# Optimization experiments

Measured on AMD Instinct MI355X. Metric: run time of the kernel, lower is better.

Reference implementation:

```python
import jax, jax.numpy as jnp
import numpy as np

NUM_HEADS = 16
EPS = 1e-5

def _lif(z, vth=1.0):
    # MyNode with fresh membrane and a single call: out = (0/tau + z >= vth)
    return (z >= vth).astype(z.dtype)

def _bn(z, g, b):
    # BatchNorm1d in train mode on (M, C, N): batch stats over (M, N)
    mu = z.mean(axis=(0, 2), keepdims=True)
    var = ((z - mu) ** 2).mean(axis=(0, 2), keepdims=True)
    return g[None, :, None] * (z - mu) * jax.lax.rsqrt(var + EPS) + b[None, :, None]

def _conv1(z, w, bias=None):
    # 1x1 Conv1d: (M, C, N) x (D, C) -> (M, D, N)
    out = jnp.einsum('mcn,dc->mdn', z, w)
    if bias is not None:
        out = out + bias[None, :, None]
    return out

def _rpb_matrix(P, N):
    # vectorized SCA_VA.compute_RPB_matrix: B[i*W+j, k*W+l] = P[(i-k)+M-1, (j-l)+M-1]
    Hs = int(round(N ** 0.5)); M = Hs + 1
    d = jnp.arange(Hs)[:, None] - jnp.arange(Hs)[None, :] + (M - 1)  # (Hs, Hs)
    Bm = P[d[:, None, :, None], d[None, :, None, :]]  # [i, j, k, l]
    return Bm.reshape(N, N)

def _sca(x, y, W, G, Bt, rpb=None):
    # shared body of SCA_AV / SCA_VA; W:(4,C,C) = [q,k,v,proj], G/Bt:(4,C) BN affine
    T, B, C, N = x.shape
    H = NUM_HEADS; D = C // H
    xf = x.reshape(T * B, C, N); yf = y.reshape(T * B, C, N)
    def branch(src, i):
        s = _lif(_bn(_conv1(src, W[i]), G[i], Bt[i]))  # (TB, C, N) binary spikes
        return s.reshape(T, B, C, N).transpose(0, 1, 3, 2).reshape(T, B, N, H, D).transpose(0, 1, 3, 2, 4)
    q = branch(xf, 0)  # (T,B,H,N,D)
    k = branch(yf, 1)
    v = branch(yf, 2)
    attn = jnp.einsum('tbhnd,tbhmd->tbhnm', q, k)  # no softmax: raw spike q@k^T
    if rpb is not None:
        attn = _lif(attn + rpb[None, None, None])  # rpb_lif (v_threshold=1.0)
    o = jnp.einsum('tbhnm,tbhmd->tbhnd', attn, v) * 0.25  # self.scale = 0.25
    o = o.transpose(0, 1, 2, 4, 3).reshape(T, B, C, N)
    o = _lif(o.reshape(T * B, C, N), 0.5)  # attn_lif v_threshold=0.5
    o = _lif(_bn(_conv1(o, W[3]), G[3], Bt[3]))  # proj_conv + proj_bn + proj_lif
    return o.reshape(T, B, C, N)

def _forward(x, y, av_w, av_g, av_b, va_w, va_g, va_b, P_rpb,
             fc1_w, fc1_b, fc2_w, fc2_b,
             m1_w, m1_b, m1_g, m1_bb, m2_w, m2_b, m2_g, m2_bb):
    T, B, C, N = x.shape
    # cross-modal spiking attention (visual->audio and audio->visual)
    x1 = x + _sca(x, y, av_w, av_g, av_b)                       # SCA_AV(x, y)
    y1 = y + _sca(y, x, va_w, va_g, va_b, rpb=_rpb_matrix(P_rpb, N))  # SCA_VA(y, x)
    # CMCI fusion: Linear on channel dim of transposed tensors, then LIF
    zx = jnp.einsum('tbcn,dc->tbdn', x1, fc1_w) + fc1_b[None, None, :, None]
    zy = jnp.einsum('tbcn,dc->tbdn', y1, fc2_w) + fc2_b[None, None, :, None]
    cur = _lif(zx + zy)  # (T,B,C,N)
    # MLPBlock: residual MLP (conv1x1 -> BN -> LIF) x 2
    cf = cur.reshape(T * B, C, N)
    h = _lif(_bn(_conv1(cf, m1_w, m1_b), m1_g, m1_bb))
    o = _lif(_bn(_conv1(h, m2_w, m2_b), m2_g, m2_bb))
    return cur + o.reshape(T, B, C, N)

def setup_inputs() -> dict:
    key = jax.random.key(0)
    ks = jax.random.split(key, 16)
    T, B, C, N = 4, 8, 256, 196
    Hd = 4 * C
    M2 = 2 * (int(N ** 0.5) + 1) - 1  # 29
    s = 0.05
    return {
        'x': jax.random.normal(ks[0], (T, B, C, N), jnp.float32),
        'y': jax.random.normal(ks[1], (T, B, C, N), jnp.float32),
        'av_w': jax.random.normal(ks[2], (4, C, C), jnp.float32) * s,
        'av_g': jnp.ones((4, C), jnp.float32),
        'av_b': jnp.zeros((4, C), jnp.float32),
        'va_w': jax.random.normal(ks[3], (4, C, C), jnp.float32) * s,
        'va_g': jnp.ones((4, C), jnp.float32),
        'va_b': jnp.zeros((4, C), jnp.float32),
        'P_rpb': jax.random.normal(ks[4], (M2, M2), jnp.float32),
        'fc1_w': jax.random.normal(ks[5], (C, C), jnp.float32) * s,
        'fc1_b': jnp.zeros((C,), jnp.float32),
        'fc2_w': jax.random.normal(ks[6], (C, C), jnp.float32) * s,
        'fc2_b': jnp.zeros((C,), jnp.float32),
        'm1_w': jax.random.normal(ks[7], (Hd, C), jnp.float32) * s,
        'm1_b': jnp.zeros((Hd,), jnp.float32),
        'm1_g': jnp.ones((Hd,), jnp.float32),
        'm1_bb': jnp.zeros((Hd,), jnp.float32),
        'm2_w': jax.random.normal(ks[8], (C, Hd), jnp.float32) * s,
        'm2_b': jnp.zeros((C,), jnp.float32),
        'm2_g': jnp.ones((C,), jnp.float32),
        'm2_bb': jnp.zeros((C,), jnp.float32),
    }

def reference(x, y, av_w, av_g, av_b, va_w, va_g, va_b, P_rpb,
              fc1_w, fc1_b, fc2_w, fc2_b,
              m1_w, m1_b, m1_g, m1_bb, m2_w, m2_b, m2_g, m2_bb):
    return _forward(x, y, av_w, av_g, av_b, va_w, va_g, va_b, P_rpb,
                    fc1_w, fc1_b, fc2_w, fc2_b,
                    m1_w, m1_b, m1_g, m1_bb, m2_w, m2_b, m2_g, m2_bb)
```

## Files before the change

kernel.cpp:

```cpp
#include <hip/hip_runtime.h>
#include <math.h>

#define TBB 32
#define CC  256
#define NN  196
#define NJ  (TBB * NN)
#define HD  1024
#define SLAB   ((size_t)TBB * CC * NN)
#define SLAB1K ((size_t)TBB * HD * NN)

struct Ptr6  { const float* p[6]; };
struct PtrM6 { float*       p[6]; };

__global__ __launch_bounds__(256) void gemm_tile(
    const float* __restrict__ W,  const float* __restrict__ In,
    const float* __restrict__ W2, const float* __restrict__ In2,
    const float* __restrict__ bias, const float* __restrict__ bias2,
    float* __restrict__ Z, int Cout, int Cin)
{
    __shared__ float As[16][64];
    __shared__ float Bs[16][64];
    const int t  = threadIdx.x;
    const int tx = t & 15, ty = t >> 4;
    const int d0 = blockIdx.x * 64;
    const int j0 = blockIdx.y * 64;

    float acc[4][4] = {{0.f}};

    const int wrow = t >> 2;
    const int wk   = (t & 3) * 4;
    const int skk  = t >> 4;
    const int sj   = (t & 15) * 4;

    size_t inoff[4];
    {
        int jb = j0 + sj;
        #pragma unroll
        for (int i = 0; i < 4; ++i) {
            int j = jb + i;
            int m = j / NN;
            int n = j - m * NN;
            inoff[i] = (size_t)m * Cin * NN + n;
        }
    }

    for (int pass = 0; pass < 2; ++pass) {
        const float* Wp = pass ? W2 : W;
        const float* Ip = pass ? In2 : In;
        if (Wp == nullptr) break;
        for (int k0 = 0; k0 < Cin; k0 += 16) {
            float4 w4 = *(const float4*)(Wp + (size_t)(d0 + wrow) * Cin + (k0 + wk));
            float bvals[4];
            #pragma unroll
            for (int i = 0; i < 4; ++i)
                bvals[i] = Ip[inoff[i] + (size_t)(k0 + skk) * NN];

            As[wk + 0][wrow] = w4.x;
            As[wk + 1][wrow] = w4.y;
            As[wk + 2][wrow] = w4.z;
            As[wk + 3][wrow] = w4.w;
            #pragma unroll
            for (int i = 0; i < 4; ++i) Bs[skk][sj + i] = bvals[i];
            __syncthreads();

            #pragma unroll
            for (int kk = 0; kk < 16; ++kk) {
                float4 a4 = *(const float4*)(&As[kk][ty * 4]);
                float4 b4 = *(const float4*)(&Bs[kk][tx * 4]);
                float ar[4] = {a4.x, a4.y, a4.z, a4.w};
                float br[4] = {b4.x, b4.y, b4.z, b4.w};
                #pragma unroll
                for (int i = 0; i < 4; ++i)
                    #pragma unroll
                    for (int jj = 0; jj < 4; ++jj)
                        acc[i][jj] = fmaf(ar[i], br[jj], acc[i][jj]);
            }
            __syncthreads();
        }
    }

    #pragma unroll
    for (int i = 0; i < 4; ++i) {
        int d = d0 + ty * 4 + i;
        float bv = 0.f;
        if (bias)  bv += bias[d];
        if (bias2) bv += bias2[d];
        #pragma unroll
        for (int jj = 0; jj < 4; ++jj) {
            int j = j0 + tx * 4 + jj;
            int m = j / NN;
            int n = j - m * NN;
            Z[(size_t)(m * Cout + d) * NN + n] = acc[i][jj] + bv;
        }
    }
}

__global__ __launch_bounds__(256) void bn_stats(
    Ptr6 Zs, Ptr6 gs, Ptr6 bs, int Cout,
    float* __restrict__ scale, float* __restrict__ shift)
{
    const int d = blockIdx.x, g = blockIdx.y, t = threadIdx.x;
    const float* Z = Zs.p[g];
    double s = 0.0, s2 = 0.0;
    for (int i = t; i < NJ; i += 256) {
        int m = i / NN, n = i - m * NN;
        double v = (double)Z[(size_t)(m * Cout + d) * NN + n];
        s += v; s2 += v * v;
    }
    __shared__ double sh[256], sh2[256];
    sh[t] = s; sh2[t] = s2;
    __syncthreads();
    for (int off = 128; off > 0; off >>= 1) {
        if (t < off) { sh[t] += sh[t + off]; sh2[t] += sh2[t + off]; }
        __syncthreads();
    }
    if (t == 0) {
        double mu  = sh[0] / (double)NJ;
        double var = sh2[0] / (double)NJ - mu * mu;
        double a   = (double)gs.p[g][d] / sqrt(var + 1e-5);
        scale[g * Cout + d] = (float)a;
        shift[g * Cout + d] = (float)((double)bs.p[g][d] - mu * a);
    }
}

__global__ __launch_bounds__(256) void bn_apply(
    Ptr6 Zs, PtrM6 Ss, const float* __restrict__ scale,
    const float* __restrict__ shift, int Cout, int total)
{
    int g = blockIdx.y;
    int idx = blockIdx.x * 256 + threadIdx.x;
    if (idx >= total) return;
    int d = (idx / NN) % Cout;
    float v = fmaf(scale[g * Cout + d], Zs.p[g][idx], shift[g * Cout + d]);
    Ss.p[g][idx] = (v >= 1.f) ? 1.f : 0.f;
}

__global__ __launch_bounds__(256) void attention_k(
    const float* __restrict__ Q, const float* __restrict__ K,
    const float* __restrict__ V, const float* __restrict__ P,
    float* __restrict__ O)
{
    const int m = blockIdx.x;
    const int h = blockIdx.y;
    const int t = threadIdx.x;
    __shared__ unsigned int qb[196], kb[196], vb[196];
    __shared__ float Pl[841];

    if (P) { for (int i = t; i < 841; i += 256) Pl[i] = P[i]; }
    if (t < 196) {
        unsigned int q = 0, k = 0, v = 0;
        size_t base = (size_t)m * CC * NN + (size_t)h * 16 * NN + t;
        #pragma unroll
        for (int dd = 0; dd < 16; ++dd) {
            size_t off = base + (size_t)dd * NN;
            if (Q[off] > 0.5f) q |= (1u << dd);
            if (K[off] > 0.5f) k |= (1u << dd);
            if (V[off] > 0.5f) v |= (1u << dd);
        }
        qb[t] = q; kb[t] = k; vb[t] = v;
    }
    __syncthreads();

    if (t < 196) {
        int acc[16] = {0};
        const int ni = t / 14, nj = t - ni * 14;
        const unsigned int qr = qb[t];
        if (P) {
            for (int mm = 0; mm < 196; ++mm) {
                int a = __popc(qr & kb[mm]);
                int mi = mm / 14, mj = mm - mi * 14;
                float sv = (float)a + Pl[(ni - mi + 14) * 29 + (nj - mj + 14)];
                if (sv >= 1.f) {
                    unsigned int vv = vb[mm];
                    #pragma unroll
                    for (int dd = 0; dd < 16; ++dd)
                        acc[dd] += (vv >> dd) & 1;
                }
            }
        } else {
            for (int mm = 0; mm < 196; ++mm) {
                int a = __popc(qr & kb[mm]);
                if (a) {
                    unsigned int vv = vb[mm];
                    #pragma unroll
                    for (int dd = 0; dd < 16; ++dd)
                        acc[dd] += ((vv >> dd) & 1) ? a : 0;
                }
            }
        }
        size_t base = (size_t)m * CC * NN + (size_t)h * 16 * NN + t;
        #pragma unroll
        for (int dd = 0; dd < 16; ++dd)
            O[base + (size_t)dd * NN] = (acc[dd] >= 2) ? 1.f : 0.f;
    }
}

__global__ __launch_bounds__(256) void add_residual2(
    const float* __restrict__ x, const float* __restrict__ y,
    const float* __restrict__ sx, const float* __restrict__ sy,
    float* __restrict__ X1, float* __restrict__ Y1)
{
    size_t i = (size_t)blockIdx.x * 256 + threadIdx.x;
    if (i >= SLAB) return;
    X1[i] = x[i] + sx[i];
    Y1[i] = y[i] + sy[i];
}

__global__ __launch_bounds__(256) void lif1(
    const float* __restrict__ Z, float* __restrict__ S, int total)
{
    int i = blockIdx.x * 256 + threadIdx.x;
    if (i >= total) return;
    S[i] = (Z[i] >= 1.f) ? 1.f : 0.f;
}

__global__ __launch_bounds__(256) void final_add(
    const float* __restrict__ cur, const float* __restrict__ o,
    float* __restrict__ out, int total)
{
    int i = blockIdx.x * 256 + threadIdx.x;
    if (i >= total) return;
    out[i] = cur[i] + o[i];
}

extern "C" void kernel_launch(void* const* d_in, const int* in_sizes, int n_in,
                              void* d_out, int out_size, void* d_ws, size_t ws_size,
                              hipStream_t stream)
{
    const float* x     = (const float*)d_in[0];
    const float* y     = (const float*)d_in[1];
    const float* av_w  = (const float*)d_in[2];
    const float* av_g  = (const float*)d_in[3];
    const float* av_b  = (const float*)d_in[4];
    const float* va_w  = (const float*)d_in[5];
    const float* va_g  = (const float*)d_in[6];
    const float* va_b  = (const float*)d_in[7];
    const float* P_rpb = (const float*)d_in[8];
    const float* fc1_w = (const float*)d_in[9];
    const float* fc1_b = (const float*)d_in[10];
    const float* fc2_w = (const float*)d_in[11];
    const float* fc2_b = (const float*)d_in[12];
    const float* m1_w  = (const float*)d_in[13];
    const float* m1_b  = (const float*)d_in[14];
    const float* m1_g  = (const float*)d_in[15];
    const float* m1_bb = (const float*)d_in[16];
    const float* m2_w  = (const float*)d_in[17];
    const float* m2_b  = (const float*)d_in[18];
    const float* m2_g  = (const float*)d_in[19];
    const float* m2_bb = (const float*)d_in[20];
    float* out = (float*)d_out;

    float* ws    = (float*)d_ws;
    float* A     = ws;
    float* Bf    = A  + 6 * SLAB;
    float* Cf    = Bf + 2 * SLAB;
    float* scale = Cf + 2 * SLAB;
    float* shift = scale + 6 * 1024;

    const size_t CC2 = (size_t)CC * CC;
    const int blocksSlab  = (int)(SLAB / 256);
    const int blocksSlab1 = (int)(SLAB1K / 256);

    const float* Wl[6] = { av_w, av_w + CC2, av_w + 2*CC2, va_w, va_w + CC2, va_w + 2*CC2 };
    const float* Il[6] = { x, y, y, y, x, x };
    for (int i = 0; i < 6; ++i)
        gemm_tile<<<dim3(CC/64, NJ/64), 256, 0, stream>>>(
            Wl[i], Il[i], nullptr, nullptr, nullptr, nullptr, A + i*SLAB, CC, CC);

    Ptr6 Zs{}, gs{}, bs{}; PtrM6 Ss{};
    const float* gl[6] = { av_g, av_g + CC, av_g + 2*CC, va_g, va_g + CC, va_g + 2*CC };
    const float* bl[6] = { av_b, av_b + CC, av_b + 2*CC, va_b, va_b + CC, va_b + 2*CC };
    for (int i = 0; i < 6; ++i) {
        Zs.p[i] = A + i*SLAB; Ss.p[i] = A + i*SLAB; gs.p[i] = gl[i]; bs.p[i] = bl[i];
    }
    bn_stats<<<dim3(CC, 6), 256, 0, stream>>>(Zs, gs, bs, CC, scale, shift);
    bn_apply<<<dim3(blocksSlab, 6), 256, 0, stream>>>(Zs, Ss, scale, shift, CC, (int)SLAB);

    attention_k<<<dim3(TBB, 16), 256, 0, stream>>>(A, A + SLAB, A + 2*SLAB, nullptr, Bf);
    attention_k<<<dim3(TBB, 16), 256, 0, stream>>>(A + 3*SLAB, A + 4*SLAB, A + 5*SLAB, P_rpb, Bf + SLAB);

    gemm_tile<<<dim3(CC/64, NJ/64), 256, 0, stream>>>(
        av_w + 3*CC2, Bf, nullptr, nullptr, nullptr, nullptr, Cf, CC, CC);
    gemm_tile<<<dim3(CC/64, NJ/64), 256, 0, stream>>>(
        va_w + 3*CC2, Bf + SLAB, nullptr, nullptr, nullptr, nullptr, Cf + SLAB, CC, CC);
    Zs.p[0] = Cf; Zs.p[1] = Cf + SLAB; Ss.p[0] = Cf; Ss.p[1] = Cf + SLAB;
    gs.p[0] = av_g + 3*CC; gs.p[1] = va_g + 3*CC;
    bs.p[0] = av_b + 3*CC; bs.p[1] = va_b + 3*CC;
    bn_stats<<<dim3(CC, 2), 256, 0, stream>>>(Zs, gs, bs, CC, scale, shift);
    bn_apply<<<dim3(blocksSlab, 2), 256, 0, stream>>>(Zs, Ss, scale, shift, CC, (int)SLAB);

    add_residual2<<<blocksSlab, 256, 0, stream>>>(x, y, Cf, Cf + SLAB, A, A + SLAB);

    gemm_tile<<<dim3(CC/64, NJ/64), 256, 0, stream>>>(
        fc1_w, A, fc2_w, A + SLAB, fc1_b, fc2_b, Bf, CC, CC);
    lif1<<<blocksSlab, 256, 0, stream>>>(Bf, Bf + SLAB, (int)SLAB);

    gemm_tile<<<dim3(HD/64, NJ/64), 256, 0, stream>>>(
        m1_w, Bf + SLAB, nullptr, nullptr, m1_b, nullptr, A, HD, CC);
    Zs.p[0] = A; Ss.p[0] = A; gs.p[0] = m1_g; bs.p[0] = m1_bb;
    bn_stats<<<dim3(HD, 1), 256, 0, stream>>>(Zs, gs, bs, HD, scale, shift);
    bn_apply<<<dim3(blocksSlab1, 1), 256, 0, stream>>>(Zs, Ss, scale, shift, HD, (int)SLAB1K);

    gemm_tile<<<dim3(CC/64, NJ/64), 256, 0, stream>>>(
        m2_w, A, nullptr, nullptr, m2_b, nullptr, Cf, CC, HD);
    Zs.p[0] = Cf; Ss.p[0] = Cf; gs.p[0] = m2_g; bs.p[0] = m2_bb;
    bn_stats<<<dim3(CC, 1), 256, 0, stream>>>(Zs, gs, bs, CC, scale, shift);
    bn_apply<<<dim3(blocksSlab, 1), 256, 0, stream>>>(Zs, Ss, scale, shift, CC, (int)SLAB);

    final_add<<<blocksSlab, 256, 0, stream>>>(Bf + SLAB, Cf, out, (int)SLAB);
}
```

Measured before the change: 669.3 us.

## Batch GEMMs, double-buffer with async LDS loads, fuse LIF and residual adds

The GEMM kernel gains double-buffered shared tiles, with B tiles loaded through global_load_lds async copies and A prefetched into registers. Six QKV GEMMs are batched into one launch via blockIdx.z, and likewise the two proj GEMMs. The LIF threshold is fused into the fc GEMM epilogue, and the residual adds are fused into a vectorized bn_apply, removing the separate add, lif and final_add kernels. The async 16-byte copy assumes each 4-element column group does not cross an image boundary (196 is divisible by 4), so the alignment is fragile. It adds complexity in exchange for fewer launches and fewer memory passes.

```diff
diff --git a/kernel.cpp b/kernel.cpp
--- a/kernel.cpp
+++ b/kernel.cpp
@@ -12,85 +12,109 @@
 struct Ptr6  { const float* p[6]; };
 struct PtrM6 { float*       p[6]; };
 
-__global__ __launch_bounds__(256) void gemm_tile(
-    const float* __restrict__ W,  const float* __restrict__ In,
-    const float* __restrict__ W2, const float* __restrict__ In2,
-    const float* __restrict__ bias, const float* __restrict__ bias2,
-    float* __restrict__ Z, int Cout, int Cin)
-{
-    __shared__ float As[16][64];
-    __shared__ float Bs[16][64];
+struct GArg {
+    const float* W;  const float* In;
+    const float* W2; const float* In2;
+    const float* bias; const float* bias2;
+    float* Z;
+};
+struct GArgs { GArg a[6]; };
+
+__device__ __forceinline__ void async_copy16(const float* gsrc, float* ldst)
+{
+    typedef __attribute__((address_space(1))) void GV;
+    typedef __attribute__((address_space(3))) void LV;
+    __builtin_amdgcn_global_load_lds((GV*)const_cast<float*>(gsrc), (LV*)ldst,
+                                     16, 0, 0);
+}
+
+__global__ __launch_bounds__(256) void gemm2(GArgs ga, int Cout, int Cin, int mode)
+{
+    __shared__ __align__(16) float As[2][16][68];
+    __shared__ __align__(16) float Bs[2][16][64];
+
+    const GArg g = ga.a[blockIdx.z];
     const int t  = threadIdx.x;
     const int tx = t & 15, ty = t >> 4;
     const int d0 = blockIdx.x * 64;
     const int j0 = blockIdx.y * 64;
-
-    float acc[4][4] = {{0.f}};
+    const int lane = t & 63, wave = t >> 6;
 
     const int wrow = t >> 2;
     const int wk   = (t & 3) * 4;
-    const int skk  = t >> 4;
-    const int sj   = (t & 15) * 4;
-
-    size_t inoff[4];
-    {
-        int jb = j0 + sj;
-        #pragma unroll
-        for (int i = 0; i < 4; ++i) {
-            int j = jb + i;
-            int m = j / NN;
-            int n = j - m * NN;
-            inoff[i] = (size_t)m * Cin * NN + n;
-        }
-    }
+
+    const int brow = wave * 4 + (lane >> 4);
+    const int bj   = j0 + (lane & 15) * 4;
+    const int bm   = bj / NN;
+    const int bn   = bj - bm * NN;
+    const size_t bbase = (size_t)bm * Cin * NN + bn;
+    float* bdst0 = &Bs[0][wave * 4][0];
+    float* bdst1 = &Bs[1][wave * 4][0];
+
+    float acc[4][4] = {{0.f}};
+    float4 wreg;
 
     for (int pass = 0; pass < 2; ++pass) {
-        const float* Wp = pass ? W2 : W;
-        const float* Ip = pass ? In2 : In;
+        const float* Wp = pass ? g.W2 : g.W;
+        const float* Ip = pass ? g.In2 : g.In;
         if (Wp == nullptr) break;
-        for (int k0 = 0; k0 < Cin; k0 += 16) {
-            float4 w4 = *(const float4*)(Wp + (size_t)(d0 + wrow) * Cin + (k0 + wk));
-            float bvals[4];
-            #pragma unroll
-            for (int i = 0; i < 4; ++i)
-                bvals[i] = Ip[inoff[i] + (size_t)(k0 + skk) * NN];
-
-            As[wk + 0][wrow] = w4.x;
-            As[wk + 1][wrow] = w4.y;
-            As[wk + 2][wrow] = w4.z;
-            As[wk + 3][wrow] = w4.w;
-            #pragma unroll
-            for (int i = 0; i < 4; ++i) Bs[skk][sj + i] = bvals[i];
-            __syncthreads();
-
+        const int nkt = Cin >> 4;
+        const size_t wbase = (size_t)(d0 + wrow) * Cin + wk;
+
+        async_copy16(Ip + bbase + (size_t)brow * NN, bdst0);
+        wreg = *(const float4*)(Wp + wbase);
+        As[0][wk + 0][wrow] = wreg.x;
+        As[0][wk + 1][wrow] = wreg.y;
+        As[0][wk + 2][wrow] = wreg.z;
+        As[0][wk + 3][wrow] = wreg.w;
+        __syncthreads();
+
+        for (int kt = 0; kt < nkt; ++kt) {
+            const int  cur  = kt & 1;
+            const int  nxt  = cur ^ 1;
+            const bool more = (kt + 1) < nkt;
+            if (more) {
+                const int k0n = (kt + 1) << 4;
+                async_copy16(Ip + bbase + (size_t)(k0n + brow) * NN,
+                             nxt ? bdst1 : bdst0);
+                wreg = *(const float4*)(Wp + wbase + k0n);
+            }
             #pragma unroll
             for (int kk = 0; kk < 16; ++kk) {
-                float4 a4 = *(const float4*)(&As[kk][ty * 4]);
-                float4 b4 = *(const float4*)(&Bs[kk][tx * 4]);
-                float ar[4] = {a4.x, a4.y, a4.z, a4.w};
-                float br[4] = {b4.x, b4.y, b4.z, b4.w};
+                const float4 a4 = *(const float4*)(&As[cur][kk][ty * 4]);
+                const float4 b4 = *(const float4*)(&Bs[cur][kk][tx * 4]);
+                const float ar[4] = {a4.x, a4.y, a4.z, a4.w};
+                const float br[4] = {b4.x, b4.y, b4.z, b4.w};
                 #pragma unroll
                 for (int i = 0; i < 4; ++i)
                     #pragma unroll
                     for (int jj = 0; jj < 4; ++jj)
                         acc[i][jj] = fmaf(ar[i], br[jj], acc[i][jj]);
             }
+            if (more) {
+                As[nxt][wk + 0][wrow] = wreg.x;
+                As[nxt][wk + 1][wrow] = wreg.y;
+                As[nxt][wk + 2][wrow] = wreg.z;
+                As[nxt][wk + 3][wrow] = wreg.w;
+            }
             __syncthreads();
         }
     }
 
     #pragma unroll
     for (int i = 0; i < 4; ++i) {
-        int d = d0 + ty * 4 + i;
+        const int d = d0 + ty * 4 + i;
         float bv = 0.f;
-        if (bias)  bv += bias[d];
-        if (bias2) bv += bias2[d];
+        if (g.bias)  bv += g.bias[d];
+        if (g.bias2) bv += g.bias2[d];
         #pragma unroll
         for (int jj = 0; jj < 4; ++jj) {
-            int j = j0 + tx * 4 + jj;
-            int m = j / NN;
-            int n = j - m * NN;
-            Z[(size_t)(m * Cout + d) * NN + n] = acc[i][jj] + bv;
+            const int j = j0 + tx * 4 + jj;
+            const int m = j / NN;
+            const int n = j - m * NN;
+            const float v = acc[i][jj] + bv;
+            g.Z[(size_t)(m * Cout + d) * NN + n] =
+                (mode == 1) ? ((v >= 1.f) ? 1.f : 0.f) : v;
         }
     }
 }
@@ -123,16 +147,28 @@
     }
 }
 
-__global__ __launch_bounds__(256) void bn_apply(
-    Ptr6 Zs, PtrM6 Ss, const float* __restrict__ scale,
-    const float* __restrict__ shift, int Cout, int total)
-{
-    int g = blockIdx.y;
-    int idx = blockIdx.x * 256 + threadIdx.x;
-    if (idx >= total) return;
-    int d = (idx / NN) % Cout;
-    float v = fmaf(scale[g * Cout + d], Zs.p[g][idx], shift[g * Cout + d]);
-    Ss.p[g][idx] = (v >= 1.f) ? 1.f : 0.f;
+__global__ __launch_bounds__(256) void bn_apply2(
+    Ptr6 Zs, PtrM6 Ss, Ptr6 Rs, const float* __restrict__ scale,
+    const float* __restrict__ shift, int Cout, int total4, int mode)
+{
+    const int gix = blockIdx.y;
+    const int i4  = blockIdx.x * 256 + threadIdx.x;
+    if (i4 >= total4) return;
+    const size_t base = (size_t)i4 * 4;
+    const int d = (int)((base / NN) % (size_t)Cout);
+    const float sc = scale[gix * Cout + d];
+    const float sh = shift[gix * Cout + d];
+    const float4 z = *(const float4*)(Zs.p[gix] + base);
+    float4 o;
+    o.x = (fmaf(sc, z.x, sh) >= 1.f) ? 1.f : 0.f;
+    o.y = (fmaf(sc, z.y, sh) >= 1.f) ? 1.f : 0.f;
+    o.z = (fmaf(sc, z.z, sh) >= 1.f) ? 1.f : 0.f;
+    o.w = (fmaf(sc, z.w, sh) >= 1.f) ? 1.f : 0.f;
+    if (mode == 1) {
+        const float4 r = *(const float4*)(Rs.p[gix] + base);
+        o.x += r.x; o.y += r.y; o.z += r.z; o.w += r.w;
+    }
+    *(float4*)(Ss.p[gix] + base) = o;
 }
 
 __global__ __launch_bounds__(256) void attention_k(
@@ -193,34 +229,6 @@
         for (int dd = 0; dd < 16; ++dd)
             O[base + (size_t)dd * NN] = (acc[dd] >= 2) ? 1.f : 0.f;
     }
-}
-
-__global__ __launch_bounds__(256) void add_residual2(
-    const float* __restrict__ x, const float* __restrict__ y,
-    const float* __restrict__ sx, const float* __restrict__ sy,
-    float* __restrict__ X1, float* __restrict__ Y1)
-{
-    size_t i = (size_t)blockIdx.x * 256 + threadIdx.x;
-    if (i >= SLAB) return;
-    X1[i] = x[i] + sx[i];
-    Y1[i] = y[i] + sy[i];
-}
-
-__global__ __launch_bounds__(256) void lif1(
-    const float* __restrict__ Z, float* __restrict__ S, int total)
-{
-    int i = blockIdx.x * 256 + threadIdx.x;
-    if (i >= total) return;
-    S[i] = (Z[i] >= 1.f) ? 1.f : 0.f;
-}
-
-__global__ __launch_bounds__(256) void final_add(
-    const float* __restrict__ cur, const float* __restrict__ o,
-    float* __restrict__ out, int total)
-{
-    int i = blockIdx.x * 256 + threadIdx.x;
-    if (i >= total) return;
-    out[i] = cur[i] + o[i];
 }
 
 extern "C" void kernel_launch(void* const* d_in, const int* in_sizes, int n_in,
@@ -258,54 +266,61 @@
     float* shift = scale + 6 * 1024;
 
     const size_t CC2 = (size_t)CC * CC;
-    const int blocksSlab  = (int)(SLAB / 256);
-    const int blocksSlab1 = (int)(SLAB1K / 256);
-
-    const float* Wl[6] = { av_w, av_w + CC2, av_w + 2*CC2, va_w, va_w + CC2, va_w + 2*CC2 };
-    const float* Il[6] = { x, y, y, y, x, x };
-    for (int i = 0; i < 6; ++i)
-        gemm_tile<<<dim3(CC/64, NJ/64), 256, 0, stream>>>(
-            Wl[i], Il[i], nullptr, nullptr, nullptr, nullptr, A + i*SLAB, CC, CC);
-
-    Ptr6 Zs{}, gs{}, bs{}; PtrM6 Ss{};
-    const float* gl[6] = { av_g, av_g + CC, av_g + 2*CC, va_g, va_g + CC, va_g + 2*CC };
-    const float* bl[6] = { av_b, av_b + CC, av_b + 2*CC, va_b, va_b + CC, va_b + 2*CC };
-    for (int i = 0; i < 6; ++i) {
-        Zs.p[i] = A + i*SLAB; Ss.p[i] = A + i*SLAB; gs.p[i] = gl[i]; bs.p[i] = bl[i];
+    const int apply256  = (int)(SLAB / 4 / 256);
+    const int apply1024 = (int)(SLAB1K / 4 / 256);
+
+    GArgs ga{};
+    {
+        const float* Wl[6] = { av_w, av_w + CC2, av_w + 2*CC2, va_w, va_w + CC2, va_w + 2*CC2 };
+        const float* Il[6] = { x, y, y, y, x, x };
+        for (int i = 0; i < 6; ++i)
+            ga.a[i] = GArg{ Wl[i], Il[i], nullptr, nullptr, nullptr, nullptr, A + i*SLAB };
+    }
+    gemm2<<<dim3(CC/64, NJ/64, 6), 256, 0, stream>>>(ga, CC, CC, 0);
+
+    Ptr6 Zs{}, gs{}, bs{}, Rs{}; PtrM6 Ss{};
+    {
+        const float* gl[6] = { av_g, av_g + CC, av_g + 2*CC, va_g, va_g + CC, va_g + 2*CC };
+        const float* bl[6] = { av_b, av_b + CC, av_b + 2*CC, va_b, va_b + CC, va_b + 2*CC };
+        for (int i = 0; i < 6; ++i) {
+            Zs.p[i] = A + i*SLAB; Ss.p[i] = A + i*SLAB; gs.p[i] = gl[i]; bs.p[i] = bl[i];
+        }
     }
     bn_stats<<<dim3(CC, 6), 256, 0, stream>>>(Zs, gs, bs, CC, scale, shift);
-    bn_apply<<<dim3(blocksSlab, 6), 256, 0, stream>>>(Zs, Ss, scale, shift, CC, (int)SLAB);
+    bn_apply2<<<dim3(apply256, 6), 256, 0, stream>>>(Zs, Ss, Rs, scale, shift, CC, (int)(SLAB/4), 0);
 
     attention_k<<<dim3(TBB, 16), 256, 0, stream>>>(A, A + SLAB, A + 2*SLAB, nullptr, Bf);
     attention_k<<<dim3(TBB, 16), 256, 0, stream>>>(A + 3*SLAB, A + 4*SLAB, A + 5*SLAB, P_rpb, Bf + SLAB);
 
-    gemm_tile<<<dim3(CC/64, NJ/64), 256, 0, stream>>>(
-        av_w + 3*CC2, Bf, nullptr, nullptr, nullptr, nullptr, Cf, CC, CC);
-    gemm_tile<<<dim3(CC/64, NJ/64), 256, 0, stream>>>(
-        va_w + 3*CC2, Bf + SLAB, nullptr, nullptr, nullptr, nullptr, Cf + SLAB, CC, CC);
-    Zs.p[0] = Cf; Zs.p[1] = Cf + SLAB; Ss.p[0] = Cf; Ss.p[1] = Cf + SLAB;
+    GArgs gc{};
+    gc.a[0] = GArg{ av_w + 3*CC2, Bf,        nullptr, nullptr, nullptr, nullptr, Cf };
+    gc.a[1] = GArg{ va_w + 3*CC2, Bf + SLAB, nullptr, nullptr, nullptr, nullptr, Cf + SLAB };
+    gemm2<<<dim3(CC/64, NJ/64, 2), 256, 0, stream>>>(gc, CC, CC, 0);
+    Zs.p[0] = Cf; Zs.p[1] = Cf + SLAB;
     gs.p[0] = av_g + 3*CC; gs.p[1] = va_g + 3*CC;
     bs.p[0] = av_b + 3*CC; bs.p[1] = va_b + 3*CC;
+    Rs.p[0] = x; Rs.p[1] = y;
+    Ss.p[0] = A; Ss.p[1] = A + SLAB;
     bn_stats<<<dim3(CC, 2), 256, 0, stream>>>(Zs, gs, bs, CC, scale, shift);
-    bn_apply<<<dim3(blocksSlab, 2), 256, 0, stream>>>(Zs, Ss, scale, shift, CC, (int)SLAB);
-
-    add_residual2<<<blocksSlab, 256, 0, stream>>>(x, y, Cf, Cf + SLAB, A, A + SLAB);
-
-    gemm_tile<<<dim3(CC/64, NJ/64), 256, 0, stream>>>(
-        fc1_w, A, fc2_w, A + SLAB, fc1_b, fc2_b, Bf, CC, CC);
-    lif1<<<blocksSlab, 256, 0, stream>>>(Bf, Bf + SLAB, (int)SLAB);
-
-    gemm_tile<<<dim3(HD/64, NJ/64), 256, 0, stream>>>(
-        m1_w, Bf + SLAB, nullptr, nullptr, m1_b, nullptr, A, HD, CC);
+    bn_apply2<<<dim3(apply256, 2), 256, 0, stream>>>(Zs, Ss, Rs, scale, shift, CC, (int)(SLAB/4), 1);
+
+    GArgs gf{};
+    gf.a[0] = GArg{ fc1_w, A, fc2_w, A + SLAB, fc1_b, fc2_b, Bf + SLAB };
+    gemm2<<<dim3(CC/64, NJ/64, 1), 256, 0, stream>>>(gf, CC, CC, 1);
+
+    GArgs g1{};
+    g1.a[0] = GArg{ m1_w, Bf + SLAB, nullptr, nullptr, m1_b, nullptr, A };
+    gemm2<<<dim3(HD/64, NJ/64, 1), 256, 0, stream>>>(g1, HD, CC, 0);
     Zs.p[0] = A; Ss.p[0] = A; gs.p[0] = m1_g; bs.p[0] = m1_bb;
     bn_stats<<<dim3(HD, 1), 256, 0, stream>>>(Zs, gs, bs, HD, scale, shift);
-    bn_apply<<<dim3(blocksSlab1, 1), 256, 0, stream>>>(Zs, Ss, scale, shift, HD, (int)SLAB1K);
-
-    gemm_tile<<<dim3(CC/64, NJ/64), 256, 0, stream>>>(
-        m2_w, A, nullptr, nullptr, m2_b, nullptr, Cf, CC, HD);
-    Zs.p[0] = Cf; Ss.p[0] = Cf; gs.p[0] = m2_g; bs.p[0] = m2_bb;
+    bn_apply2<<<dim3(apply1024, 1), 256, 0, stream>>>(Zs, Ss, Rs, scale, shift, HD, (int)(SLAB1K/4), 0);
+
+    GArgs g2{};
+    g2.a[0] = GArg{ m2_w, A, nullptr, nullptr, m2_b, nullptr, Cf };
+    gemm2<<<dim3(CC/64, NJ/64, 1), 256, 0, stream>>>(g2, CC, HD, 0);
+    Zs.p[0] = Cf; gs.p[0] = m2_g; bs.p[0] = m2_bb;
+    Rs.p[0] = Bf + SLAB;
+    Ss.p[0] = out;
     bn_stats<<<dim3(CC, 1), 256, 0, stream>>>(Zs, gs, bs, CC, scale, shift);
-    bn_apply<<<dim3(blocksSlab, 1), 256, 0, stream>>>(Zs, Ss, scale, shift, CC, (int)SLAB);
-
-    final_add<<<blocksSlab, 256, 0, stream>>>(Bf + SLAB, Cf, out, (int)SLAB);
-}
+    bn_apply2<<<dim3(apply256, 1), 256, 0, stream>>>(Zs, Ss, Rs, scale, shift, CC, (int)(SLAB/4), 1);
+}
```

After: 541.5 us. -19.1%, faster.
